# Performance work log

Measured on AMD Instinct MI355X. Metric: run time of the kernel, lower is better.

## Reference

```python
import jax, jax.numpy as jnp
import numpy as np

N_NODES = 50000


def gcn_conv(x, W, b, edge_index, n_nodes):
    """torch_geometric GCNConv: linear -> symmetric-normalized scatter-add with self-loops."""
    h = x @ W  # [N, out]
    src = jnp.concatenate([edge_index[0], jnp.arange(n_nodes)])  # add self-loops
    dst = jnp.concatenate([edge_index[1], jnp.arange(n_nodes)])
    deg = jax.ops.segment_sum(jnp.ones_like(dst, dtype=h.dtype), dst, num_segments=n_nodes)
    dinv = jnp.where(deg > 0, jax.lax.rsqrt(deg), 0.0)  # deg^-1/2, inf -> 0
    norm = dinv[src] * dinv[dst]                         # [E+N]
    msg = h[src] * norm[:, None]                         # gather + scale
    out = jax.ops.segment_sum(msg, dst, num_segments=n_nodes)  # scatter-add
    return out + b


def setup_inputs() -> dict:
    key = jax.random.key(0)
    k1, k2, k3, k4, k5, k6 = jax.random.split(key, 6)
    nhid, nfeat = 128, 256
    E = 800000
    x = jax.random.normal(k1, (N_NODES, nhid), dtype=jnp.float32)
    edge_index = jax.random.randint(k2, (2, E), 0, N_NODES, dtype=jnp.int64)
    s1 = 1.0 / np.sqrt(nhid)
    W1 = jax.random.uniform(k3, (nhid, nhid), jnp.float32, -s1, s1)
    b1 = jnp.zeros((nhid,), jnp.float32)
    W2 = jax.random.uniform(k4, (nhid, nfeat), jnp.float32, -s1, s1)
    b2 = jnp.zeros((nfeat,), jnp.float32)
    return {"x": x, "edge_index": edge_index, "W1": W1, "b1": b1, "W2": W2, "b2": b2}


def reference(x, edge_index, W1, b1, W2, b2):
    # eval mode: dropout is identity
    h = jax.nn.relu(gcn_conv(x, W1, b1, edge_index, N_NODES))
    out = jax.nn.relu(gcn_conv(h, W2, b2, edge_index, N_NODES))
    return out
```

## Files before the change

### kernel.cpp

```cpp
#include <hip/hip_runtime.h>


typedef __attribute__((ext_vector_type(8))) _Float16 half8;
typedef __attribute__((ext_vector_type(4))) _Float16 half4v;
typedef __attribute__((ext_vector_type(4))) float floatx4;

#define BSHIFT 7
#define BNODES 128
#define BCAP   4096

__global__ __launch_bounds__(256) void scatter_conv_kernel(const int* __restrict__ src,
                                                           const int* __restrict__ dst,
                                                           int* __restrict__ bucket_fill,
                                                           unsigned* __restrict__ bucketed,
                                                           const float* __restrict__ W1,
                                                           const float* __restrict__ W2,
                                                           _Float16* __restrict__ wt1,
                                                           _Float16* __restrict__ wt2,
                                                           int E, int chunk, int NB) {
    int t = threadIdx.x;
    if (blockIdx.x >= 256) {
        int idx = (blockIdx.x - 256) * 256 + t;
        if (idx < 128 * 128) {
            int nn = idx >> 7, k = idx & 127;
            wt1[idx] = (_Float16)W1[k * 128 + nn];
        } else if (idx < (128 + 256) * 128) {
            int j = idx - 128 * 128;
            int nn = j >> 7, k = j & 127;
            wt2[j] = (_Float16)W2[k * 256 + nn];
        }
        return;
    }
    extern __shared__ int sh[];
    int* hist = sh;
    int* base_loc = sh + NB;
    int* cur2 = sh + 2 * NB;
    for (int i = t; i < NB; i += 256) { hist[i] = 0; cur2[i] = 0; }
    __syncthreads();
    int cbeg = blockIdx.x * chunk;
    int cend = min(E, cbeg + chunk);
    for (int e = cbeg + t; e < cend; e += 256)
        atomicAdd(&hist[dst[e] >> BSHIFT], 1);
    __syncthreads();
    for (int i = t; i < NB; i += 256) {
        int c = hist[i];
        base_loc[i] = c ? atomicAdd(&bucket_fill[i], c) : 0;
    }
    __syncthreads();
    for (int e = cbeg + t; e < cend; e += 256) {
        int d = dst[e];
        int bkt = d >> BSHIFT;
        int r = atomicAdd(&cur2[bkt], 1);
        bucketed[(size_t)bkt * BCAP + base_loc[bkt] + r] =
            (unsigned)src[e] | ((unsigned)(d & (BNODES - 1)) << 16);
    }
}

__global__ __launch_bounds__(256) void build_kernel(const unsigned* __restrict__ bucketed,
                                                    const int* __restrict__ bucket_fill,
                                                    const float* __restrict__ x,
                                                    int* __restrict__ rowstart,
                                                    int* __restrict__ rowend,
                                                    float* __restrict__ dinv,
                                                    int* __restrict__ csr,
                                                    _Float16* __restrict__ xs,
                                                    int N, int NB) {
    __shared__ int deg_loc[BNODES];
    __shared__ int tmp[BNODES];
    __shared__ int cur_loc[BNODES];
    __shared__ float dinv_loc[BNODES];
    __shared__ int lcsr[BCAP];
    int t = threadIdx.x;
    int b = blockIdx.x;
    int n0 = b << BSHIFT;
    int nodes_in = min(BNODES, N - n0);
    size_t wbase = (size_t)b * BCAP;
    int cnt = bucket_fill[b];

    if (t < BNODES) deg_loc[t] = 0;
    __syncthreads();
    for (int e = t; e < cnt; e += 256)
        atomicAdd(&deg_loc[bucketed[wbase + e] >> 16], 1);
    __syncthreads();
    if (t < BNODES) tmp[t] = deg_loc[t];
    __syncthreads();
    for (int off = 1; off < BNODES; off <<= 1) {
        int v = 0;
        if (t < BNODES && t >= off) v = tmp[t - off];
        __syncthreads();
        if (t < BNODES) tmp[t] += v;
        __syncthreads();
    }
    if (t < BNODES) {
        int loc0 = tmp[t] - deg_loc[t];
        cur_loc[t] = loc0;
        float dv = rsqrtf((float)(deg_loc[t] + 1));
        dinv_loc[t] = dv;
        if (t < nodes_in) {
            rowstart[n0 + t] = (int)wbase + loc0;
            rowend[n0 + t] = (int)wbase + loc0 + deg_loc[t];
            dinv[n0 + t] = dv;
        }
    }
    __syncthreads();
    for (int e = t; e < cnt; e += 256) {
        unsigned u2 = bucketed[wbase + e];
        int pos = atomicAdd(&cur_loc[u2 >> 16], 1);
        lcsr[pos] = (int)(u2 & 0xFFFFu);
    }
    __syncthreads();
    {
        int qw = t >> 4;
        int ql = t & 15;
        for (int row = qw; row < nodes_in; row += 16) {
            int deg = deg_loc[row];
            if (deg < 2 || deg > 64) continue;
            int rb = tmp[row] - deg;
            int keys[4], ranks[4];
            int ne = 0;
#pragma unroll 4
            for (int e = ql; e < deg; e += 16) {
                int key = lcsr[rb + e];
                int rank = 0;
                for (int j = 0; j < deg; j++) {
                    int v = lcsr[rb + j];
                    rank += (v < key) || (v == key && j < e);
                }
                keys[ne] = key; ranks[ne] = rank; ne++;
            }
            for (int i = 0; i < ne; i++)
                lcsr[rb + ranks[i]] = keys[i];
        }
    }
    __syncthreads();
    for (int e = t; e < cnt; e += 256)
        csr[wbase + e] = lcsr[e];
    int total4 = nodes_in * 32;
    const float4* x4 = (const float4*)(x + (size_t)n0 * 128);
    for (int i = t; i < total4; i += 256) {
        int row = i >> 5;
        float dv = dinv_loc[row];
        float4 v = x4[i];
        half4v h;
        h[0] = (_Float16)(v.x * dv); h[1] = (_Float16)(v.y * dv);
        h[2] = (_Float16)(v.z * dv); h[3] = (_Float16)(v.w * dv);
        *(half4v*)(xs + (size_t)n0 * 128 + (size_t)i * 4) = h;
    }
}

__global__ __launch_bounds__(256) void agg128_kernel(const _Float16* __restrict__ g,
                                                     const int* __restrict__ rowstart,
                                                     const int* __restrict__ rowend,
                                                     const float* __restrict__ dinv,
                                                     const int* __restrict__ csr,
                                                     _Float16* __restrict__ out, int n) {
    int wave = (blockIdx.x * blockDim.x + threadIdx.x) >> 6;
    int lane = threadIdx.x & 63;
    int q = lane >> 4, l16 = lane & 15;
    int node = wave * 4 + q;
    if (node >= n) return;
    int beg = rowstart[node], end = rowend[node];

    float a[8];
    {
        half8 v = *(const half8*)(g + (size_t)node * 128 + l16 * 8);
#pragma unroll
        for (int j = 0; j < 8; j++) a[j] = (float)v[j];
    }
    int e = beg;
    for (; e + 7 < end; e += 8) {
        int u0 = csr[e],     u1 = csr[e + 1], u2 = csr[e + 2], u3 = csr[e + 3];
        int u4 = csr[e + 4], u5 = csr[e + 5], u6 = csr[e + 6], u7 = csr[e + 7];
        half8 v0 = *(const half8*)(g + (size_t)u0 * 128 + l16 * 8);
        half8 v1 = *(const half8*)(g + (size_t)u1 * 128 + l16 * 8);
        half8 v2 = *(const half8*)(g + (size_t)u2 * 128 + l16 * 8);
        half8 v3 = *(const half8*)(g + (size_t)u3 * 128 + l16 * 8);
        half8 v4 = *(const half8*)(g + (size_t)u4 * 128 + l16 * 8);
        half8 v5 = *(const half8*)(g + (size_t)u5 * 128 + l16 * 8);
        half8 v6 = *(const half8*)(g + (size_t)u6 * 128 + l16 * 8);
        half8 v7 = *(const half8*)(g + (size_t)u7 * 128 + l16 * 8);
#pragma unroll
        for (int j = 0; j < 8; j++)
            a[j] += (((float)v0[j] + (float)v1[j]) + ((float)v2[j] + (float)v3[j])) +
                    (((float)v4[j] + (float)v5[j]) + ((float)v6[j] + (float)v7[j]));
    }
    for (; e + 3 < end; e += 4) {
        int u0 = csr[e], u1 = csr[e + 1], u2 = csr[e + 2], u3 = csr[e + 3];
        half8 v0 = *(const half8*)(g + (size_t)u0 * 128 + l16 * 8);
        half8 v1 = *(const half8*)(g + (size_t)u1 * 128 + l16 * 8);
        half8 v2 = *(const half8*)(g + (size_t)u2 * 128 + l16 * 8);
        half8 v3 = *(const half8*)(g + (size_t)u3 * 128 + l16 * 8);
#pragma unroll
        for (int j = 0; j < 8; j++)
            a[j] += ((float)v0[j] + (float)v1[j]) + ((float)v2[j] + (float)v3[j]);
    }
    for (; e < end; e++) {
        int u = csr[e];
        half8 v = *(const half8*)(g + (size_t)u * 128 + l16 * 8);
#pragma unroll
        for (int j = 0; j < 8; j++) a[j] += (float)v[j];
    }
    float dv = dinv[node];
    half8 o;
#pragma unroll
    for (int j = 0; j < 8; j++) o[j] = (_Float16)(a[j] * dv);
    *(half8*)(out + (size_t)node * 128 + l16 * 8) = o;
}

template <bool HALF_OUT>
__global__ __launch_bounds__(256) void gemm_kernel(const _Float16* __restrict__ A,
                                                   const _Float16* __restrict__ Bt,
                                                   const float* __restrict__ bias,
                                                   const float* __restrict__ dinv,
                                                   void* __restrict__ outp,
                                                   int n, int nout) {
    __shared__ _Float16 As[128][136];
    __shared__ _Float16 Bs[128][136];
    int t = threadIdx.x;
    int row0 = blockIdx.x * 128;
    int col0 = blockIdx.y * 128;

#pragma unroll
    for (int i = 0; i < 8; i++) {
        int c = i * 256 + t;
        int r = c >> 4, seg = c & 15;
        int gr = row0 + r;
        if (gr >= n) gr = n - 1;
        uint4 v = *(const uint4*)(A + (size_t)gr * 128 + seg * 8);
        *(uint4*)(&As[r][seg * 8]) = v;
    }
#pragma unroll
    for (int i = 0; i < 8; i++) {
        int c = i * 256 + t;
        int r = c >> 4, seg = c & 15;
        uint4 v = *(const uint4*)(Bt + (size_t)(col0 + r) * 128 + seg * 8);
        *(uint4*)(&Bs[r][seg * 8]) = v;
    }
    __syncthreads();

    int wid = t >> 6, lane = t & 63;
    int wm = wid >> 1, wn = wid & 1;
    int quad = lane >> 4, l16 = lane & 15;

    floatx4 acc[4][4];
#pragma unroll
    for (int mt = 0; mt < 4; mt++)
#pragma unroll
        for (int nt = 0; nt < 4; nt++) acc[mt][nt] = (floatx4){0.f, 0.f, 0.f, 0.f};

#pragma unroll
    for (int ks = 0; ks < 4; ks++) {
        int k0 = ks * 32 + quad * 8;
        half8 a[4], b[4];
#pragma unroll
        for (int mt = 0; mt < 4; mt++)
            a[mt] = *(const half8*)(&As[wm * 64 + mt * 16 + l16][k0]);
#pragma unroll
        for (int nt = 0; nt < 4; nt++)
            b[nt] = *(const half8*)(&Bs[wn * 64 + nt * 16 + l16][k0]);
#pragma unroll
        for (int mt = 0; mt < 4; mt++)
#pragma unroll
            for (int nt = 0; nt < 4; nt++)
                acc[mt][nt] = __builtin_amdgcn_mfma_f32_16x16x32_f16(a[mt], b[nt], acc[mt][nt], 0, 0, 0);
    }

#pragma unroll
    for (int mt = 0; mt < 4; mt++) {
        int rbase = row0 + wm * 64 + mt * 16 + quad * 4;
#pragma unroll
        for (int reg = 0; reg < 4; reg++) {
            int r = rbase + reg;
            if (r < n) {
                float dv = HALF_OUT ? dinv[r] : 1.f;
#pragma unroll
                for (int nt = 0; nt < 4; nt++) {
                    int cc = col0 + wn * 64 + nt * 16 + l16;
                    float val = fmaxf(acc[mt][nt][reg] + bias[cc], 0.f);
                    if (HALF_OUT)
                        ((_Float16*)outp)[(size_t)r * nout + cc] = (_Float16)(val * dv);
                    else
                        ((float*)outp)[(size_t)r * nout + cc] = val;
                }
            }
        }
    }
}

extern "C" void kernel_launch(void* const* d_in, const int* in_sizes, int n_in,
                              void* d_out, int out_size, void* d_ws, size_t ws_size,
                              hipStream_t stream) {
    const float* x  = (const float*)d_in[0];
    const int*   ei = (const int*)d_in[1];
    const float* W1 = (const float*)d_in[2];
    const float* b1 = (const float*)d_in[3];
    const float* W2 = (const float*)d_in[4];
    const float* b2 = (const float*)d_in[5];
    float* out = (float*)d_out;

    int N = in_sizes[0] / 128;
    int E = in_sizes[1] / 2;
    const int* src = ei;
    const int* dst = ei + E;
    int NB = (N + BNODES - 1) >> BSHIFT;

    char* w = (char*)d_ws;
    size_t off = 0;
    auto alloc = [&](size_t bytes) -> char* {
        char* p = w + off;
        off = (off + bytes + 255) & ~(size_t)255;
        return p;
    };
    int*      bucket_fill = (int*)alloc((size_t)NB * 4);
    unsigned* bucketed    = (unsigned*)alloc((size_t)NB * BCAP * 4);
    int*      rowstart    = (int*)alloc((size_t)N * 4);
    int*      rowend      = (int*)alloc((size_t)N * 4);
    float*    dinv        = (float*)alloc((size_t)N * 4);
    int*      csr         = (int*)alloc((size_t)NB * BCAP * 4);
    _Float16* wt1         = (_Float16*)alloc((size_t)128 * 128 * 2);
    _Float16* wt2         = (_Float16*)alloc((size_t)256 * 128 * 2);
    _Float16* xs          = (_Float16*)alloc((size_t)N * 128 * 2);
    _Float16* q1          = (_Float16*)alloc((size_t)N * 128 * 2);
    _Float16* p2          = (_Float16*)alloc((size_t)N * 128 * 2);
    _Float16* q2          = (_Float16*)alloc((size_t)N * 128 * 2);

    int chunk = (E + 255) / 256;
    size_t lds3 = (size_t)NB * 12;

    hipMemsetAsync(bucket_fill, 0, (size_t)NB * 4, stream);
    hipLaunchKernelGGL(scatter_conv_kernel, dim3(256 + 192), dim3(256), lds3, stream,
                       src, dst, bucket_fill, bucketed, W1, W2, wt1, wt2, E, chunk, NB);
    hipLaunchKernelGGL(build_kernel, dim3(NB), dim3(256), 0, stream,
                       bucketed, bucket_fill, x, rowstart, rowend, dinv, csr, xs, N, NB);

    int gbm = (N + 127) / 128;
    int nwave = (N + 3) / 4;
    int nb_agg = (nwave * 64 + 255) / 256;
    hipLaunchKernelGGL(agg128_kernel, dim3(nb_agg), dim3(256), 0, stream, xs, rowstart, rowend, dinv, csr, q1, N);
    hipLaunchKernelGGL((gemm_kernel<true>), dim3(gbm, 1), dim3(256), 0, stream, q1, wt1, b1, dinv, (void*)p2, N, 128);
    hipLaunchKernelGGL(agg128_kernel, dim3(nb_agg), dim3(256), 0, stream, p2, rowstart, rowend, dinv, csr, q2, N);
    hipLaunchKernelGGL((gemm_kernel<false>), dim3(gbm, 2), dim3(256), 0, stream, q2, wt2, b2, dinv, (void*)out, N, 256);
}
```

Baseline: 231.2 us.

## Compute degrees with global atomics, split x scaling into own kernel, add 64-row GEMM

Per-node degrees are now counted in the scatter kernel using global atomics on a zeroed deg array. This removes the per-bucket degree histogram pass from build_kernel. The x-to-fp16 scaling moves out of build_kernel into a separate, fully parallel xs_kernel, so the 391-block build kernel does less serial work. The first GEMM gets a dedicated 64-row-tile kernel that launches twice as many blocks, giving better occupancy over N=50000. The cost is one extra launch and 800k global atomics that may contend.

```diff
diff --git a/kernel.cpp b/kernel.cpp
--- a/kernel.cpp
+++ b/kernel.cpp
@@ -13,6 +13,7 @@
                                                            const int* __restrict__ dst,
                                                            int* __restrict__ bucket_fill,
                                                            unsigned* __restrict__ bucketed,
+                                                           int* __restrict__ deg,
                                                            const float* __restrict__ W1,
                                                            const float* __restrict__ W2,
                                                            _Float16* __restrict__ wt1,
@@ -39,8 +40,11 @@
     __syncthreads();
     int cbeg = blockIdx.x * chunk;
     int cend = min(E, cbeg + chunk);
-    for (int e = cbeg + t; e < cend; e += 256)
-        atomicAdd(&hist[dst[e] >> BSHIFT], 1);
+    for (int e = cbeg + t; e < cend; e += 256) {
+        int d = dst[e];
+        atomicAdd(&hist[d >> BSHIFT], 1);
+        atomicAdd(&deg[d], 1);
+    }
     __syncthreads();
     for (int i = t; i < NB; i += 256) {
         int c = hist[i];
@@ -56,19 +60,32 @@
     }
 }
 
+__global__ __launch_bounds__(256) void xs_kernel(const float* __restrict__ x,
+                                                 const int* __restrict__ deg,
+                                                 float* __restrict__ dinv,
+                                                 _Float16* __restrict__ xs, int N) {
+    int row = blockIdx.x * 8 + (threadIdx.x >> 5);
+    int l32 = threadIdx.x & 31;
+    if (row >= N) return;
+    float dv = rsqrtf((float)(deg[row] + 1));
+    if (l32 == 0) dinv[row] = dv;
+    float4 v = *(const float4*)(x + (size_t)row * 128 + l32 * 4);
+    half4v h;
+    h[0] = (_Float16)(v.x * dv); h[1] = (_Float16)(v.y * dv);
+    h[2] = (_Float16)(v.z * dv); h[3] = (_Float16)(v.w * dv);
+    *(half4v*)(xs + (size_t)row * 128 + l32 * 4) = h;
+}
+
 __global__ __launch_bounds__(256) void build_kernel(const unsigned* __restrict__ bucketed,
                                                     const int* __restrict__ bucket_fill,
-                                                    const float* __restrict__ x,
+                                                    const int* __restrict__ deg,
                                                     int* __restrict__ rowstart,
                                                     int* __restrict__ rowend,
-                                                    float* __restrict__ dinv,
                                                     int* __restrict__ csr,
-                                                    _Float16* __restrict__ xs,
                                                     int N, int NB) {
     __shared__ int deg_loc[BNODES];
     __shared__ int tmp[BNODES];
     __shared__ int cur_loc[BNODES];
-    __shared__ float dinv_loc[BNODES];
     __shared__ int lcsr[BCAP];
     int t = threadIdx.x;
     int b = blockIdx.x;
@@ -77,10 +94,7 @@
     size_t wbase = (size_t)b * BCAP;
     int cnt = bucket_fill[b];
 
-    if (t < BNODES) deg_loc[t] = 0;
-    __syncthreads();
-    for (int e = t; e < cnt; e += 256)
-        atomicAdd(&deg_loc[bucketed[wbase + e] >> 16], 1);
+    if (t < BNODES) deg_loc[t] = (t < nodes_in) ? deg[n0 + t] : 0;
     __syncthreads();
     if (t < BNODES) tmp[t] = deg_loc[t];
     __syncthreads();
@@ -94,12 +108,9 @@
     if (t < BNODES) {
         int loc0 = tmp[t] - deg_loc[t];
         cur_loc[t] = loc0;
-        float dv = rsqrtf((float)(deg_loc[t] + 1));
-        dinv_loc[t] = dv;
         if (t < nodes_in) {
             rowstart[n0 + t] = (int)wbase + loc0;
             rowend[n0 + t] = (int)wbase + loc0 + deg_loc[t];
-            dinv[n0 + t] = dv;
         }
     }
     __syncthreads();
@@ -113,16 +124,16 @@
         int qw = t >> 4;
         int ql = t & 15;
         for (int row = qw; row < nodes_in; row += 16) {
-            int deg = deg_loc[row];
-            if (deg < 2 || deg > 64) continue;
-            int rb = tmp[row] - deg;
+            int deg_r = deg_loc[row];
+            if (deg_r < 2 || deg_r > 64) continue;
+            int rb = tmp[row] - deg_r;
             int keys[4], ranks[4];
             int ne = 0;
 #pragma unroll 4
-            for (int e = ql; e < deg; e += 16) {
+            for (int e = ql; e < deg_r; e += 16) {
                 int key = lcsr[rb + e];
                 int rank = 0;
-                for (int j = 0; j < deg; j++) {
+                for (int j = 0; j < deg_r; j++) {
                     int v = lcsr[rb + j];
                     rank += (v < key) || (v == key && j < e);
                 }
@@ -135,17 +146,6 @@
     __syncthreads();
     for (int e = t; e < cnt; e += 256)
         csr[wbase + e] = lcsr[e];
-    int total4 = nodes_in * 32;
-    const float4* x4 = (const float4*)(x + (size_t)n0 * 128);
-    for (int i = t; i < total4; i += 256) {
-        int row = i >> 5;
-        float dv = dinv_loc[row];
-        float4 v = x4[i];
-        half4v h;
-        h[0] = (_Float16)(v.x * dv); h[1] = (_Float16)(v.y * dv);
-        h[2] = (_Float16)(v.z * dv); h[3] = (_Float16)(v.w * dv);
-        *(half4v*)(xs + (size_t)n0 * 128 + (size_t)i * 4) = h;
-    }
 }
 
 __global__ __launch_bounds__(256) void agg128_kernel(const _Float16* __restrict__ g,
@@ -207,12 +207,72 @@
     *(half8*)(out + (size_t)node * 128 + l16 * 8) = o;
 }
 
-template <bool HALF_OUT>
+__global__ __launch_bounds__(256) void gemm64_kernel(const _Float16* __restrict__ A,
+                                                     const _Float16* __restrict__ Bt,
+                                                     const float* __restrict__ bias,
+                                                     const float* __restrict__ dinv,
+                                                     _Float16* __restrict__ outp,
+                                                     int n) {
+    __shared__ _Float16 As[64][136];
+    __shared__ _Float16 Bs[128][136];
+    int t = threadIdx.x;
+    int row0 = blockIdx.x * 64;
+
+#pragma unroll
+    for (int i = 0; i < 4; i++) {
+        int c = i * 256 + t;
+        int r = c >> 4, seg = c & 15;
+        int gr = row0 + r;
+        if (gr >= n) gr = n - 1;
+        uint4 v = *(const uint4*)(A + (size_t)gr * 128 + seg * 8);
+        *(uint4*)(&As[r][seg * 8]) = v;
+    }
+#pragma unroll
+    for (int i = 0; i < 8; i++) {
+        int c = i * 256 + t;
+        int r = c >> 4, seg = c & 15;
+        uint4 v = *(const uint4*)(Bt + (size_t)r * 128 + seg * 8);
+        *(uint4*)(&Bs[r][seg * 8]) = v;
+    }
+    __syncthreads();
+
+    int wid = t >> 6, lane = t & 63;
+    int quad = lane >> 4, l16 = lane & 15;
+
+    floatx4 acc[8];
+#pragma unroll
+    for (int nt = 0; nt < 8; nt++) acc[nt] = (floatx4){0.f, 0.f, 0.f, 0.f};
+
+#pragma unroll
+    for (int ks = 0; ks < 4; ks++) {
+        int k0 = ks * 32 + quad * 8;
+        half8 a = *(const half8*)(&As[wid * 16 + l16][k0]);
+#pragma unroll
+        for (int nt = 0; nt < 8; nt++) {
+            half8 b = *(const half8*)(&Bs[nt * 16 + l16][k0]);
+            acc[nt] = __builtin_amdgcn_mfma_f32_16x16x32_f16(a, b, acc[nt], 0, 0, 0);
+        }
+    }
+
+#pragma unroll
+    for (int reg = 0; reg < 4; reg++) {
+        int r = row0 + wid * 16 + quad * 4 + reg;
+        if (r < n) {
+            float dv = dinv[r];
+#pragma unroll
+            for (int nt = 0; nt < 8; nt++) {
+                int cc = nt * 16 + l16;
+                float val = fmaxf(acc[nt][reg] + bias[cc], 0.f);
+                outp[(size_t)r * 128 + cc] = (_Float16)(val * dv);
+            }
+        }
+    }
+}
+
 __global__ __launch_bounds__(256) void gemm_kernel(const _Float16* __restrict__ A,
                                                    const _Float16* __restrict__ Bt,
                                                    const float* __restrict__ bias,
-                                                   const float* __restrict__ dinv,
-                                                   void* __restrict__ outp,
+                                                   float* __restrict__ outp,
                                                    int n, int nout) {
     __shared__ _Float16 As[128][136];
     __shared__ _Float16 Bs[128][136];
@@ -272,15 +332,10 @@
         for (int reg = 0; reg < 4; reg++) {
             int r = rbase + reg;
             if (r < n) {
-                float dv = HALF_OUT ? dinv[r] : 1.f;
 #pragma unroll
                 for (int nt = 0; nt < 4; nt++) {
                     int cc = col0 + wn * 64 + nt * 16 + l16;
-                    float val = fmaxf(acc[mt][nt][reg] + bias[cc], 0.f);
-                    if (HALF_OUT)
-                        ((_Float16*)outp)[(size_t)r * nout + cc] = (_Float16)(val * dv);
-                    else
-                        ((float*)outp)[(size_t)r * nout + cc] = val;
+                    outp[(size_t)r * nout + cc] = fmaxf(acc[mt][nt][reg] + bias[cc], 0.f);
                 }
             }
         }
@@ -312,6 +367,7 @@
         return p;
     };
     int*      bucket_fill = (int*)alloc((size_t)NB * 4);
+    int*      deg         = (int*)alloc((size_t)N * 4);
     unsigned* bucketed    = (unsigned*)alloc((size_t)NB * BCAP * 4);
     int*      rowstart    = (int*)alloc((size_t)N * 4);
     int*      rowend      = (int*)alloc((size_t)N * 4);
@@ -327,17 +383,20 @@
     int chunk = (E + 255) / 256;
     size_t lds3 = (size_t)NB * 12;
 
-    hipMemsetAsync(bucket_fill, 0, (size_t)NB * 4, stream);
+    hipMemsetAsync(bucket_fill, 0, (size_t)((char*)bucketed - (char*)bucket_fill), stream);
     hipLaunchKernelGGL(scatter_conv_kernel, dim3(256 + 192), dim3(256), lds3, stream,
-                       src, dst, bucket_fill, bucketed, W1, W2, wt1, wt2, E, chunk, NB);
+                       src, dst, bucket_fill, bucketed, deg, W1, W2, wt1, wt2, E, chunk, NB);
+    hipLaunchKernelGGL(xs_kernel, dim3((N + 7) / 8), dim3(256), 0, stream,
+                       x, deg, dinv, xs, N);
     hipLaunchKernelGGL(build_kernel, dim3(NB), dim3(256), 0, stream,
-                       bucketed, bucket_fill, x, rowstart, rowend, dinv, csr, xs, N, NB);
-
-    int gbm = (N + 127) / 128;
+                       bucketed, bucket_fill, deg, rowstart, rowend, csr, N, NB);
+
     int nwave = (N + 3) / 4;
     int nb_agg = (nwave * 64 + 255) / 256;
+    int gbm64 = (N + 63) / 64;
+    int gbm = (N + 127) / 128;
     hipLaunchKernelGGL(agg128_kernel, dim3(nb_agg), dim3(256), 0, stream, xs, rowstart, rowend, dinv, csr, q1, N);
-    hipLaunchKernelGGL((gemm_kernel<true>), dim3(gbm, 1), dim3(256), 0, stream, q1, wt1, b1, dinv, (void*)p2, N, 128);
+    hipLaunchKernelGGL(gemm64_kernel, dim3(gbm64), dim3(256), 0, stream, q1, wt1, b1, dinv, p2, N);
     hipLaunchKernelGGL(agg128_kernel, dim3(nb_agg), dim3(256), 0, stream, p2, rowstart, rowend, dinv, csr, q2, N);
-    hipLaunchKernelGGL((gemm_kernel<false>), dim3(gbm, 2), dim3(256), 0, stream, q2, wt2, b2, dinv, (void*)out, N, 256);
-}
+    hipLaunchKernelGGL(gemm_kernel, dim3(gbm, 2), dim3(256), 0, stream, q2, wt2, b2, out, N, 256);
+}
```

New measurement: 255.0 us. +10.3%, slower.

## Stage edge scatter in LDS for contiguous bucket writes; split x scaling kernel

Applied to the files above, without the earlier changes.

The edge-bucketing kernel now does a local prefix sum over bucket counts, sorts each block's edges by bucket in shared memory, and then writes them out in bucket-contiguous runs, so global writes are no longer scattered one per edge. The build kernel copies each bucket into LDS once instead of reading global memory twice. The x-to-fp16 scaling moves out of the per-bucket build kernel into its own fully parallel kernel. This adds an extra launch and a larger static LDS footprint, and it assumes at most 400 buckets and 3200 edges per chunk.

```diff
diff --git a/kernel.cpp b/kernel.cpp
--- a/kernel.cpp
+++ b/kernel.cpp
@@ -8,6 +8,8 @@
 #define BSHIFT 7
 #define BNODES 128
 #define BCAP   4096
+#define NBMAX  400
+#define BCHUNK 3200
 
 __global__ __launch_bounds__(256) void scatter_conv_kernel(const int* __restrict__ src,
                                                            const int* __restrict__ dst,
@@ -31,14 +33,17 @@
         }
         return;
     }
-    extern __shared__ int sh[];
-    int* hist = sh;
-    int* base_loc = sh + NB;
-    int* cur2 = sh + 2 * NB;
+    __shared__ int hist[NBMAX];
+    __shared__ int base_loc[NBMAX];
+    __shared__ int cur2[NBMAX];
+    __shared__ int locx[512];
+    __shared__ unsigned estage[BCHUNK];
+    __shared__ unsigned short bkt16[BCHUNK];
     for (int i = t; i < NB; i += 256) { hist[i] = 0; cur2[i] = 0; }
     __syncthreads();
     int cbeg = blockIdx.x * chunk;
     int cend = min(E, cbeg + chunk);
+    int cntc = cend - cbeg;
     for (int e = cbeg + t; e < cend; e += 256)
         atomicAdd(&hist[dst[e] >> BSHIFT], 1);
     __syncthreads();
@@ -46,30 +51,52 @@
         int c = hist[i];
         base_loc[i] = c ? atomicAdd(&bucket_fill[i], c) : 0;
     }
-    __syncthreads();
+    for (int i = t; i < 512; i += 256) locx[i] = (i < NB) ? hist[i] : 0;
+    __syncthreads();
+    for (int off = 1; off < 512; off <<= 1) {
+        int i0 = t, i1 = t + 256;
+        int v0 = (i0 >= off) ? locx[i0 - off] : 0;
+        int v1 = (i1 >= off) ? locx[i1 - off] : 0;
+        __syncthreads();
+        locx[i0] += v0; locx[i1] += v1;
+        __syncthreads();
+    }
+    {
+        int e0 = (t < NB) ? locx[t] - hist[t] : 0;
+        int e1 = (t + 256 < NB) ? locx[t + 256] - hist[t + 256] : 0;
+        __syncthreads();
+        if (t < NB) locx[t] = e0;
+        if (t + 256 < NB) locx[t + 256] = e1;
+        __syncthreads();
+    }
     for (int e = cbeg + t; e < cend; e += 256) {
         int d = dst[e];
         int bkt = d >> BSHIFT;
         int r = atomicAdd(&cur2[bkt], 1);
-        bucketed[(size_t)bkt * BCAP + base_loc[bkt] + r] =
-            (unsigned)src[e] | ((unsigned)(d & (BNODES - 1)) << 16);
+        int idx = locx[bkt] + r;
+        estage[idx] = (unsigned)src[e] | ((unsigned)(d & (BNODES - 1)) << 16);
+        bkt16[idx] = (unsigned short)bkt;
+    }
+    __syncthreads();
+    for (int i = t; i < cntc; i += 256) {
+        int bkt = bkt16[i];
+        int pos = base_loc[bkt] + (i - locx[bkt]);
+        bucketed[(size_t)bkt * BCAP + pos] = estage[i];
     }
 }
 
 __global__ __launch_bounds__(256) void build_kernel(const unsigned* __restrict__ bucketed,
                                                     const int* __restrict__ bucket_fill,
-                                                    const float* __restrict__ x,
                                                     int* __restrict__ rowstart,
                                                     int* __restrict__ rowend,
                                                     float* __restrict__ dinv,
                                                     int* __restrict__ csr,
-                                                    _Float16* __restrict__ xs,
                                                     int N, int NB) {
+    __shared__ unsigned raw[BCAP];
+    __shared__ int lcsr[BCAP];
     __shared__ int deg_loc[BNODES];
     __shared__ int tmp[BNODES];
     __shared__ int cur_loc[BNODES];
-    __shared__ float dinv_loc[BNODES];
-    __shared__ int lcsr[BCAP];
     int t = threadIdx.x;
     int b = blockIdx.x;
     int n0 = b << BSHIFT;
@@ -77,10 +104,11 @@
     size_t wbase = (size_t)b * BCAP;
     int cnt = bucket_fill[b];
 
+    for (int e = t; e < cnt; e += 256) raw[e] = bucketed[wbase + e];
     if (t < BNODES) deg_loc[t] = 0;
     __syncthreads();
     for (int e = t; e < cnt; e += 256)
-        atomicAdd(&deg_loc[bucketed[wbase + e] >> 16], 1);
+        atomicAdd(&deg_loc[raw[e] >> 16], 1);
     __syncthreads();
     if (t < BNODES) tmp[t] = deg_loc[t];
     __syncthreads();
@@ -95,7 +123,6 @@
         int loc0 = tmp[t] - deg_loc[t];
         cur_loc[t] = loc0;
         float dv = rsqrtf((float)(deg_loc[t] + 1));
-        dinv_loc[t] = dv;
         if (t < nodes_in) {
             rowstart[n0 + t] = (int)wbase + loc0;
             rowend[n0 + t] = (int)wbase + loc0 + deg_loc[t];
@@ -104,7 +131,7 @@
     }
     __syncthreads();
     for (int e = t; e < cnt; e += 256) {
-        unsigned u2 = bucketed[wbase + e];
+        unsigned u2 = raw[e];
         int pos = atomicAdd(&cur_loc[u2 >> 16], 1);
         lcsr[pos] = (int)(u2 & 0xFFFFu);
     }
@@ -113,16 +140,16 @@
         int qw = t >> 4;
         int ql = t & 15;
         for (int row = qw; row < nodes_in; row += 16) {
-            int deg = deg_loc[row];
-            if (deg < 2 || deg > 64) continue;
-            int rb = tmp[row] - deg;
+            int deg_r = deg_loc[row];
+            if (deg_r < 2 || deg_r > 64) continue;
+            int rb = tmp[row] - deg_r;
             int keys[4], ranks[4];
             int ne = 0;
 #pragma unroll 4
-            for (int e = ql; e < deg; e += 16) {
+            for (int e = ql; e < deg_r; e += 16) {
                 int key = lcsr[rb + e];
                 int rank = 0;
-                for (int j = 0; j < deg; j++) {
+                for (int j = 0; j < deg_r; j++) {
                     int v = lcsr[rb + j];
                     rank += (v < key) || (v == key && j < e);
                 }
@@ -135,17 +162,20 @@
     __syncthreads();
     for (int e = t; e < cnt; e += 256)
         csr[wbase + e] = lcsr[e];
-    int total4 = nodes_in * 32;
-    const float4* x4 = (const float4*)(x + (size_t)n0 * 128);
-    for (int i = t; i < total4; i += 256) {
-        int row = i >> 5;
-        float dv = dinv_loc[row];
-        float4 v = x4[i];
-        half4v h;
-        h[0] = (_Float16)(v.x * dv); h[1] = (_Float16)(v.y * dv);
-        h[2] = (_Float16)(v.z * dv); h[3] = (_Float16)(v.w * dv);
-        *(half4v*)(xs + (size_t)n0 * 128 + (size_t)i * 4) = h;
-    }
+}
+
+__global__ __launch_bounds__(256) void xs_kernel(const float* __restrict__ x,
+                                                 const float* __restrict__ dinv,
+                                                 _Float16* __restrict__ xs, int N) {
+    int row = blockIdx.x * 8 + (threadIdx.x >> 5);
+    int l32 = threadIdx.x & 31;
+    if (row >= N) return;
+    float dv = dinv[row];
+    float4 v = *(const float4*)(x + (size_t)row * 128 + l32 * 4);
+    half4v h;
+    h[0] = (_Float16)(v.x * dv); h[1] = (_Float16)(v.y * dv);
+    h[2] = (_Float16)(v.z * dv); h[3] = (_Float16)(v.w * dv);
+    *(half4v*)(xs + (size_t)row * 128 + l32 * 4) = h;
 }
 
 __global__ __launch_bounds__(256) void agg128_kernel(const _Float16* __restrict__ g,
@@ -325,17 +355,18 @@
     _Float16* q2          = (_Float16*)alloc((size_t)N * 128 * 2);
 
     int chunk = (E + 255) / 256;
-    size_t lds3 = (size_t)NB * 12;
 
     hipMemsetAsync(bucket_fill, 0, (size_t)NB * 4, stream);
-    hipLaunchKernelGGL(scatter_conv_kernel, dim3(256 + 192), dim3(256), lds3, stream,
+    hipLaunchKernelGGL(scatter_conv_kernel, dim3(256 + 192), dim3(256), 0, stream,
                        src, dst, bucket_fill, bucketed, W1, W2, wt1, wt2, E, chunk, NB);
     hipLaunchKernelGGL(build_kernel, dim3(NB), dim3(256), 0, stream,
-                       bucketed, bucket_fill, x, rowstart, rowend, dinv, csr, xs, N, NB);
-
-    int gbm = (N + 127) / 128;
+                       bucketed, bucket_fill, rowstart, rowend, dinv, csr, N, NB);
+    hipLaunchKernelGGL(xs_kernel, dim3((N + 7) / 8), dim3(256), 0, stream,
+                       x, dinv, xs, N);
+
     int nwave = (N + 3) / 4;
     int nb_agg = (nwave * 64 + 255) / 256;
+    int gbm = (N + 127) / 128;
     hipLaunchKernelGGL(agg128_kernel, dim3(nb_agg), dim3(256), 0, stream, xs, rowstart, rowend, dinv, csr, q1, N);
     hipLaunchKernelGGL((gemm_kernel<true>), dim3(gbm, 1), dim3(256), 0, stream, q1, wt1, b1, dinv, (void*)p2, N, 128);
     hipLaunchKernelGGL(agg128_kernel, dim3(nb_agg), dim3(256), 0, stream, p2, rowstart, rowend, dinv, csr, q2, N);
```

After: 230.9 us. No clear change (-0.1%).
